# Performance work log

Measured on AMD Instinct MI355X. Metric: run time of the kernel, lower is better.

## Reference

```python
import jax, jax.numpy as jnp
import numpy as np

E = 8        # num_experts
D_IN = 512   # num_inputs
H = 256      # num_neurons_expert
T = 64       # num_neurons_tower
B = 16384    # batch


def setup_inputs() -> dict:
    key = jax.random.key(0)
    ks = jax.random.split(key, 7)
    s_in = 1.0 / np.sqrt(D_IN)
    s_h = 1.0 / np.sqrt(H)
    return {
        "xv": jax.random.normal(ks[0], (B, D_IN), dtype=jnp.float32),
        # expert weights stacked: torch Linear weight is (out,in) -> (E, H, D_IN)
        "We": jax.random.uniform(ks[1], (E, H, D_IN), jnp.float32, -s_in, s_in),
        "be": jax.random.uniform(ks[2], (E, H), jnp.float32, -s_in, s_in),
        "Wg": jax.random.uniform(ks[3], (E, D_IN), jnp.float32, -s_in, s_in),
        "bg": jax.random.uniform(ks[4], (E,), jnp.float32, -s_in, s_in),
        "Wt": jax.random.uniform(ks[5], (T, H), jnp.float32, -s_h, s_h),
        "bt": jax.random.uniform(ks[6], (T,), jnp.float32, -s_h, s_h),
    }


def reference(xv, We, be, Wg, bg, Wt, bt):
    # All experts as one batched GEMM: [B,D] x [E,H,D] -> [B,E,H]
    experts = jax.nn.relu(jnp.einsum("bd,ehd->beh", xv, We) + be[None, :, :])
    # Dropout is identity in eval mode.
    gate = jax.nn.softmax(xv @ Wg.T + bg, axis=1)            # [B,E]
    combined = jnp.einsum("beh,be->bh", experts, gate)        # [B,H]
    out = jax.nn.sigmoid(combined @ Wt.T + bt)                # [B,T]
    return out
```

## Files before the change

### kernel.cpp

```cpp
#include <hip/hip_runtime.h>
#include <hip/hip_bf16.h>
#include <stdint.h>

typedef unsigned short u16;
typedef __bf16 bf16x8 __attribute__((ext_vector_type(8)));
typedef float f32x4 __attribute__((ext_vector_type(4)));

#define LDS_A_USH 8192
#define LDS_B_USH 16384

__device__ __forceinline__ void glds16(const void* g, void* l) {
  __builtin_amdgcn_global_load_lds(
      (const __attribute__((address_space(1))) unsigned int*)g,
      (__attribute__((address_space(3))) unsigned int*)l, 16, 0, 0);
}

__device__ __forceinline__ u16 f2bf(float f) {
  unsigned int u = __builtin_bit_cast(unsigned int, f);
  u += 0x7fffu + ((u >> 16) & 1u);
  return (u16)(u >> 16);
}

__global__ __launch_bounds__(256) void prep_kernel(
    const float* __restrict__ xv, const float* __restrict__ We,
    const float* __restrict__ Wg, const float* __restrict__ bg,
    const float* __restrict__ Wt,
    u16* __restrict__ xv_bf, u16* __restrict__ We_bf,
    u16* __restrict__ Wt_bf, float* __restrict__ gate) {
  const int bx = blockIdx.x;
  if (bx < 4096) {
    const int wid = threadIdx.x >> 6, lane = threadIdx.x & 63;
    const int row = bx * 4 + wid;
    const float* xr = xv + (row << 9) + lane * 8;
    float4 x0 = *(const float4*)xr;
    float4 x1 = *(const float4*)(xr + 4);
    uint4 o;
    o.x = (unsigned)f2bf(x0.x) | ((unsigned)f2bf(x0.y) << 16);
    o.y = (unsigned)f2bf(x0.z) | ((unsigned)f2bf(x0.w) << 16);
    o.z = (unsigned)f2bf(x1.x) | ((unsigned)f2bf(x1.y) << 16);
    o.w = (unsigned)f2bf(x1.z) | ((unsigned)f2bf(x1.w) << 16);
    *(uint4*)(xv_bf + (row << 9) + lane * 8) = o;
    float s[8];
#pragma unroll
    for (int e = 0; e < 8; e++) {
      const float* wg = Wg + (e << 9) + lane * 8;
      float4 w0 = *(const float4*)wg;
      float4 w1 = *(const float4*)(wg + 4);
      s[e] = x0.x * w0.x + x0.y * w0.y + x0.z * w0.z + x0.w * w0.w +
             x1.x * w1.x + x1.y * w1.y + x1.z * w1.z + x1.w * w1.w;
    }
#pragma unroll
    for (int e = 0; e < 8; e++) {
#pragma unroll
      for (int off = 32; off > 0; off >>= 1) s[e] += __shfl_xor(s[e], off);
      s[e] += bg[e];
    }
    float mx = s[0];
#pragma unroll
    for (int e = 1; e < 8; e++) mx = fmaxf(mx, s[e]);
    float p[8], sum = 0.f;
#pragma unroll
    for (int e = 0; e < 8; e++) { p[e] = __expf(s[e] - mx); sum += p[e]; }
    float inv = 1.f / sum;
    if (lane == 0) {
      float4 g0 = {p[0] * inv, p[1] * inv, p[2] * inv, p[3] * inv};
      float4 g1 = {p[4] * inv, p[5] * inv, p[6] * inv, p[7] * inv};
      *(float4*)(gate + row * 8) = g0;
      *(float4*)(gate + row * 8 + 4) = g1;
    }
  } else {
    const int base = (bx - 4096) * 2048 + threadIdx.x * 8;
    const float* src;
    u16* dst;
    if (base < 1048576) { src = We + base; dst = We_bf + base; }
    else { src = Wt + (base - 1048576); dst = Wt_bf + (base - 1048576); }
    float4 a = *(const float4*)src;
    float4 b = *(const float4*)(src + 4);
    uint4 o;
    o.x = (unsigned)f2bf(a.x) | ((unsigned)f2bf(a.y) << 16);
    o.y = (unsigned)f2bf(a.z) | ((unsigned)f2bf(a.w) << 16);
    o.z = (unsigned)f2bf(b.x) | ((unsigned)f2bf(b.y) << 16);
    o.w = (unsigned)f2bf(b.z) | ((unsigned)f2bf(b.w) << 16);
    *(uint4*)dst = o;
  }
}

__global__ __launch_bounds__(256, 2) void moe_main(
    const u16* __restrict__ xv_bf, const u16* __restrict__ We_bf,
    const float* __restrict__ be, const float* __restrict__ gate,
    const u16* __restrict__ Wt_bf, float* __restrict__ part) {
  __shared__ u16 lds[LDS_A_USH + LDS_B_USH];

  const int bx = blockIdx.x;
  const int mb = bx >> 1;
  const int hb = bx & 1;
  const int m0 = mb << 6;
  const int tid = threadIdx.x;
  const int lane = tid & 63;
  const int wid = tid >> 6;
  const int wm = wid >> 1;
  const int wn = wid & 1;
  const int l15 = lane & 15;
  const int l4 = lane >> 4;

  f32x4 comb[2][4];
#pragma unroll
  for (int mt = 0; mt < 2; mt++)
#pragma unroll
    for (int nt = 0; nt < 4; nt++) comb[mt][nt] = {0.f, 0.f, 0.f, 0.f};

  for (int e = 0; e < 8; e++) {
    f32x4 acc[2][4];
#pragma unroll
    for (int mt = 0; mt < 2; mt++)
#pragma unroll
      for (int nt = 0; nt < 4; nt++) acc[mt][nt] = {0.f, 0.f, 0.f, 0.f};

    const u16* Wb = We_bf + (e << 17);
    for (int kc = 0; kc < 4; kc++) {
      __syncthreads();
      const int kofs = kc << 7;
#pragma unroll
      for (int r = 0; r < 4; r++) {
        int gi = r * 256 + tid;
        int m = gi >> 4, s = gi & 15;
        int g = (s & 8) | ((s & 7) ^ (m & 7));
        glds16(xv_bf + ((m0 + m) << 9) + kofs + (g << 3), &lds[gi << 3]);
      }
#pragma unroll
      for (int r = 0; r < 8; r++) {
        int gi = r * 256 + tid;
        int n = gi >> 4, s = gi & 15;
        int g = (s & 8) | ((s & 7) ^ (n & 7));
        glds16(Wb + (((hb << 7) + n) << 9) + kofs + (g << 3),
               &lds[LDS_A_USH + (gi << 3)]);
      }
      __syncthreads();
#pragma unroll
      for (int ks = 0; ks < 4; ks++) {
        const int gg = ks * 4 + l4;
        bf16x8 af[2], bfr[4];
#pragma unroll
        for (int mt = 0; mt < 2; mt++) {
          int row = wm * 32 + mt * 16 + l15;
          int slot = (gg & 8) | ((gg & 7) ^ (row & 7));
          af[mt] = *(const bf16x8*)&lds[(row << 7) + (slot << 3)];
        }
#pragma unroll
        for (int nt = 0; nt < 4; nt++) {
          int n = wn * 64 + nt * 16 + l15;
          int slot = (gg & 8) | ((gg & 7) ^ (n & 7));
          bfr[nt] = *(const bf16x8*)&lds[LDS_A_USH + (n << 7) + (slot << 3)];
        }
#pragma unroll
        for (int mt = 0; mt < 2; mt++)
#pragma unroll
          for (int nt = 0; nt < 4; nt++)
            acc[mt][nt] = __builtin_amdgcn_mfma_f32_16x16x32_bf16(
                af[mt], bfr[nt], acc[mt][nt], 0, 0, 0);
      }
    }
    float bev[4];
#pragma unroll
    for (int nt = 0; nt < 4; nt++)
      bev[nt] = be[(e << 8) + (hb << 7) + wn * 64 + nt * 16 + l15];
#pragma unroll
    for (int mt = 0; mt < 2; mt++) {
#pragma unroll
      for (int i = 0; i < 4; i++) {
        float g = gate[((m0 + wm * 32 + mt * 16 + l4 * 4 + i) << 3) + e];
#pragma unroll
        for (int nt = 0; nt < 4; nt++)
          comb[mt][nt][i] += g * fmaxf(acc[mt][nt][i] + bev[nt], 0.f);
      }
    }
  }

  __syncthreads();
#pragma unroll
  for (int mt = 0; mt < 2; mt++)
#pragma unroll
    for (int i = 0; i < 4; i++) {
      int row = wm * 32 + mt * 16 + l4 * 4 + i;
#pragma unroll
      for (int nt = 0; nt < 4; nt++) {
        int col = wn * 64 + nt * 16 + l15;
        __bf16 v = (__bf16)comb[mt][nt][i];
        lds[row * 136 + col] = __builtin_bit_cast(u16, v);
      }
    }
  __syncthreads();
  f32x4 tacc[4];
#pragma unroll
  for (int nt = 0; nt < 4; nt++) tacc[nt] = {0.f, 0.f, 0.f, 0.f};
  const u16* WtB = Wt_bf + (hb << 7);
#pragma unroll
  for (int kc = 0; kc < 4; kc++) {
    int ko = kc * 32 + l4 * 8;
    bf16x8 aT = *(const bf16x8*)&lds[(wid * 16 + l15) * 136 + ko];
#pragma unroll
    for (int nt = 0; nt < 4; nt++) {
      bf16x8 bT = *(const bf16x8*)&WtB[(nt * 16 + l15) * 256 + ko];
      tacc[nt] = __builtin_amdgcn_mfma_f32_16x16x32_bf16(aT, bT, tacc[nt], 0, 0, 0);
    }
  }
  float* pout = part + hb * 1048576;
#pragma unroll
  for (int nt = 0; nt < 4; nt++)
#pragma unroll
    for (int i = 0; i < 4; i++) {
      int grow = m0 + wid * 16 + l4 * 4 + i;
      pout[grow * 64 + nt * 16 + l15] = tacc[nt][i];
    }
}

__global__ __launch_bounds__(256) void finish_kernel(
    const float* __restrict__ part, const float* __restrict__ bt,
    float* __restrict__ out) {
  const int idx = (blockIdx.x * 256 + threadIdx.x) << 2;
  float4 a = *(const float4*)(part + idx);
  float4 b = *(const float4*)(part + 1048576 + idx);
  float4 c = *(const float4*)(bt + (idx & 63));
  float4 r;
  r.x = 1.f / (1.f + __expf(-(a.x + b.x + c.x)));
  r.y = 1.f / (1.f + __expf(-(a.y + b.y + c.y)));
  r.z = 1.f / (1.f + __expf(-(a.z + b.z + c.z)));
  r.w = 1.f / (1.f + __expf(-(a.w + b.w + c.w)));
  *(float4*)(out + idx) = r;
}

extern "C" void kernel_launch(void* const* d_in, const int* in_sizes, int n_in,
                              void* d_out, int out_size, void* d_ws, size_t ws_size,
                              hipStream_t stream) {
  const float* xv = (const float*)d_in[0];
  const float* We = (const float*)d_in[1];
  const float* be = (const float*)d_in[2];
  const float* Wg = (const float*)d_in[3];
  const float* bg = (const float*)d_in[4];
  const float* Wt = (const float*)d_in[5];
  const float* bt = (const float*)d_in[6];

  char* ws = (char*)d_ws;
  u16* xv_bf = (u16*)ws;
  u16* We_bf = (u16*)(ws + 16777216);
  u16* Wt_bf = (u16*)(ws + 18874368);
  float* gate = (float*)(ws + 18907136);
  float* part = (float*)(ws + 19431424);

  prep_kernel<<<4616, 256, 0, stream>>>(xv, We, Wg, bg, Wt, xv_bf, We_bf, Wt_bf, gate);
  moe_main<<<512, 256, 0, stream>>>(xv_bf, We_bf, be, gate, Wt_bf, part);
  finish_kernel<<<1024, 256, 0, stream>>>(part, bt, (float*)d_out);
}
```

Measured before the change: 154.2 us.

## Fuse gating, x conversion and tower output into a single double-buffered MoE kernel

Removes the separate xv-to-bf16 pass and the finish kernel. Each 512-thread block now holds its 64-row x tile in registers as bf16, computes the gate on the MFMA units with a split hi/lo bf16 scheme, and double-buffers the expert weight chunks in LDS. The block also computes all 256 hidden columns and applies the tower bias and sigmoid directly. This cuts global traffic for the bf16 x copy, the gate array and the partial sums, and overlaps weight loads with compute. In exchange the grid shrinks to 256 blocks with heavy register use, which may limit occupancy on a 256-CU GPU.

```diff
diff --git a/kernel.cpp b/kernel.cpp
--- a/kernel.cpp
+++ b/kernel.cpp
@@ -6,8 +6,6 @@
 typedef __bf16 bf16x8 __attribute__((ext_vector_type(8)));
 typedef float f32x4 __attribute__((ext_vector_type(4)));
 
-#define LDS_A_USH 8192
-#define LDS_B_USH 16384
 
 __device__ __forceinline__ void glds16(const void* g, void* l) {
   __builtin_amdgcn_global_load_lds(
@@ -21,59 +19,16 @@
   return (u16)(u >> 16);
 }
 
-__global__ __launch_bounds__(256) void prep_kernel(
-    const float* __restrict__ xv, const float* __restrict__ We,
-    const float* __restrict__ Wg, const float* __restrict__ bg,
-    const float* __restrict__ Wt,
-    u16* __restrict__ xv_bf, u16* __restrict__ We_bf,
-    u16* __restrict__ Wt_bf, float* __restrict__ gate) {
+__global__ __launch_bounds__(256) void prep_w(
+    const float* __restrict__ We, const float* __restrict__ Wt,
+    const float* __restrict__ Wg,
+    u16* __restrict__ We_bf, u16* __restrict__ Wt_bf,
+    u16* __restrict__ Wg_hi, u16* __restrict__ Wg_lo) {
   const int bx = blockIdx.x;
-  if (bx < 4096) {
-    const int wid = threadIdx.x >> 6, lane = threadIdx.x & 63;
-    const int row = bx * 4 + wid;
-    const float* xr = xv + (row << 9) + lane * 8;
-    float4 x0 = *(const float4*)xr;
-    float4 x1 = *(const float4*)(xr + 4);
-    uint4 o;
-    o.x = (unsigned)f2bf(x0.x) | ((unsigned)f2bf(x0.y) << 16);
-    o.y = (unsigned)f2bf(x0.z) | ((unsigned)f2bf(x0.w) << 16);
-    o.z = (unsigned)f2bf(x1.x) | ((unsigned)f2bf(x1.y) << 16);
-    o.w = (unsigned)f2bf(x1.z) | ((unsigned)f2bf(x1.w) << 16);
-    *(uint4*)(xv_bf + (row << 9) + lane * 8) = o;
-    float s[8];
-#pragma unroll
-    for (int e = 0; e < 8; e++) {
-      const float* wg = Wg + (e << 9) + lane * 8;
-      float4 w0 = *(const float4*)wg;
-      float4 w1 = *(const float4*)(wg + 4);
-      s[e] = x0.x * w0.x + x0.y * w0.y + x0.z * w0.z + x0.w * w0.w +
-             x1.x * w1.x + x1.y * w1.y + x1.z * w1.z + x1.w * w1.w;
-    }
-#pragma unroll
-    for (int e = 0; e < 8; e++) {
-#pragma unroll
-      for (int off = 32; off > 0; off >>= 1) s[e] += __shfl_xor(s[e], off);
-      s[e] += bg[e];
-    }
-    float mx = s[0];
-#pragma unroll
-    for (int e = 1; e < 8; e++) mx = fmaxf(mx, s[e]);
-    float p[8], sum = 0.f;
-#pragma unroll
-    for (int e = 0; e < 8; e++) { p[e] = __expf(s[e] - mx); sum += p[e]; }
-    float inv = 1.f / sum;
-    if (lane == 0) {
-      float4 g0 = {p[0] * inv, p[1] * inv, p[2] * inv, p[3] * inv};
-      float4 g1 = {p[4] * inv, p[5] * inv, p[6] * inv, p[7] * inv};
-      *(float4*)(gate + row * 8) = g0;
-      *(float4*)(gate + row * 8 + 4) = g1;
-    }
-  } else {
-    const int base = (bx - 4096) * 2048 + threadIdx.x * 8;
-    const float* src;
-    u16* dst;
-    if (base < 1048576) { src = We + base; dst = We_bf + base; }
-    else { src = Wt + (base - 1048576); dst = Wt_bf + (base - 1048576); }
+  if (bx < 520) {
+    const float* src; u16* dst;
+    if (bx < 512) { int base = bx * 2048 + threadIdx.x * 8; src = We + base; dst = We_bf + base; }
+    else { int base = (bx - 512) * 2048 + threadIdx.x * 8; src = Wt + base; dst = Wt_bf + base; }
     float4 a = *(const float4*)src;
     float4 b = *(const float4*)(src + 4);
     uint4 o;
@@ -82,26 +37,118 @@
     o.z = (unsigned)f2bf(b.x) | ((unsigned)f2bf(b.y) << 16);
     o.w = (unsigned)f2bf(b.z) | ((unsigned)f2bf(b.w) << 16);
     *(uint4*)dst = o;
-  }
-}
-
-__global__ __launch_bounds__(256, 2) void moe_main(
-    const u16* __restrict__ xv_bf, const u16* __restrict__ We_bf,
-    const float* __restrict__ be, const float* __restrict__ gate,
-    const u16* __restrict__ Wt_bf, float* __restrict__ part) {
-  __shared__ u16 lds[LDS_A_USH + LDS_B_USH];
-
-  const int bx = blockIdx.x;
-  const int mb = bx >> 1;
-  const int hb = bx & 1;
-  const int m0 = mb << 6;
+  } else {
+    int base = (bx - 520) * 2048 + threadIdx.x * 8;
+    float x[8];
+    float4 a = *(const float4*)(Wg + base);
+    float4 b = *(const float4*)(Wg + base + 4);
+    x[0]=a.x; x[1]=a.y; x[2]=a.z; x[3]=a.w; x[4]=b.x; x[5]=b.y; x[6]=b.z; x[7]=b.w;
+    u16 h[8], l[8];
+#pragma unroll
+    for (int j = 0; j < 8; j++) {
+      h[j] = f2bf(x[j]);
+      float hf = __builtin_bit_cast(float, ((unsigned)h[j]) << 16);
+      l[j] = f2bf(x[j] - hf);
+    }
+    uint4 oh, ol;
+    oh.x = (unsigned)h[0] | ((unsigned)h[1] << 16);
+    oh.y = (unsigned)h[2] | ((unsigned)h[3] << 16);
+    oh.z = (unsigned)h[4] | ((unsigned)h[5] << 16);
+    oh.w = (unsigned)h[6] | ((unsigned)h[7] << 16);
+    ol.x = (unsigned)l[0] | ((unsigned)l[1] << 16);
+    ol.y = (unsigned)l[2] | ((unsigned)l[3] << 16);
+    ol.z = (unsigned)l[4] | ((unsigned)l[5] << 16);
+    ol.w = (unsigned)l[6] | ((unsigned)l[7] << 16);
+    *(uint4*)(Wg_hi + base) = oh;
+    *(uint4*)(Wg_lo + base) = ol;
+  }
+}
+
+__device__ __forceinline__ void stage_chunk(const u16* __restrict__ We_bf,
+                                            u16* ldsbuf, int t, int tid) {
+  const int e_ = t >> 2, kc_ = t & 3;
+  const u16* src = We_bf + (e_ << 17) + (kc_ << 7);
+#pragma unroll
+  for (int r = 0; r < 8; r++) {
+    int gi = r * 512 + tid;
+    int n = gi >> 4, s = gi & 15;
+    int g = (s & 8) | ((s & 7) ^ (n & 7));
+    glds16(src + (n << 9) + (g << 3), ldsbuf + (gi << 3));
+  }
+}
+
+__global__ __launch_bounds__(512, 2) void moe_main(
+    const float* __restrict__ xv, const u16* __restrict__ We_bf,
+    const float* __restrict__ be, const float* __restrict__ bg,
+    const u16* __restrict__ Wg_hi, const u16* __restrict__ Wg_lo,
+    const u16* __restrict__ Wt_bf, const float* __restrict__ bt,
+    float* __restrict__ out) {
+  __shared__ u16 lds[65536];
+
   const int tid = threadIdx.x;
   const int lane = tid & 63;
   const int wid = tid >> 6;
-  const int wm = wid >> 1;
-  const int wn = wid & 1;
+  const int wm = wid >> 2;
+  const int wn = wid & 3;
   const int l15 = lane & 15;
   const int l4 = lane >> 4;
+  const int m0 = blockIdx.x << 6;
+
+  stage_chunk(We_bf, lds, 0, tid);
+
+  bf16x8 ah[2][16];
+  f32x4 gacc[2] = {{0.f,0.f,0.f,0.f},{0.f,0.f,0.f,0.f}};
+  const int esrc = l15 & 7;
+#pragma unroll
+  for (int mt = 0; mt < 2; mt++) {
+    bf16x8 alo[16];
+#pragma unroll
+    for (int ks = 0; ks < 16; ks++) {
+      const float* ap = xv + ((m0 + wm * 32 + mt * 16 + l15) << 9) + ks * 32 + l4 * 8;
+      float4 xa = *(const float4*)ap;
+      float4 xb = *(const float4*)(ap + 4);
+      float x[8];
+      x[0]=xa.x; x[1]=xa.y; x[2]=xa.z; x[3]=xa.w; x[4]=xb.x; x[5]=xb.y; x[6]=xb.z; x[7]=xb.w;
+      bf16x8 hv, lv;
+#pragma unroll
+      for (int j = 0; j < 8; j++) {
+        u16 hb_ = f2bf(x[j]);
+        float hf = __builtin_bit_cast(float, ((unsigned)hb_) << 16);
+        hv[j] = __builtin_bit_cast(__bf16, hb_);
+        lv[j] = __builtin_bit_cast(__bf16, f2bf(x[j] - hf));
+      }
+      ah[mt][ks] = hv;
+      alo[ks] = lv;
+    }
+#pragma unroll
+    for (int ks = 0; ks < 16; ks++) {
+      bf16x8 wh = *(const bf16x8*)(Wg_hi + (esrc << 9) + ks * 32 + l4 * 8);
+      bf16x8 wl = *(const bf16x8*)(Wg_lo + (esrc << 9) + ks * 32 + l4 * 8);
+      gacc[mt] = __builtin_amdgcn_mfma_f32_16x16x32_bf16(ah[mt][ks], wh, gacc[mt], 0, 0, 0);
+      gacc[mt] = __builtin_amdgcn_mfma_f32_16x16x32_bf16(alo[ks],    wh, gacc[mt], 0, 0, 0);
+      gacc[mt] = __builtin_amdgcn_mfma_f32_16x16x32_bf16(ah[mt][ks], wl, gacc[mt], 0, 0, 0);
+    }
+  }
+  float gv[2][4];
+  {
+    float bgv = bg[esrc];
+#pragma unroll
+    for (int mt = 0; mt < 2; mt++)
+#pragma unroll
+      for (int i = 0; i < 4; i++) {
+        float z = gacc[mt][i] + bgv;
+        float mx = z;
+        mx = fmaxf(mx, __shfl_xor(mx, 1));
+        mx = fmaxf(mx, __shfl_xor(mx, 2));
+        mx = fmaxf(mx, __shfl_xor(mx, 4));
+        float p = __expf(z - mx);
+        float s = p;
+        s += __shfl_xor(s, 1);
+        s += __shfl_xor(s, 2);
+        s += __shfl_xor(s, 4);
+        gv[mt][i] = p / s;
+      }
+  }
 
   f32x4 comb[2][4];
 #pragma unroll
@@ -109,6 +156,7 @@
 #pragma unroll
     for (int nt = 0; nt < 4; nt++) comb[mt][nt] = {0.f, 0.f, 0.f, 0.f};
 
+#pragma unroll 1
   for (int e = 0; e < 8; e++) {
     f32x4 acc[2][4];
 #pragma unroll
@@ -116,64 +164,43 @@
 #pragma unroll
       for (int nt = 0; nt < 4; nt++) acc[mt][nt] = {0.f, 0.f, 0.f, 0.f};
 
-    const u16* Wb = We_bf + (e << 17);
+#pragma unroll
     for (int kc = 0; kc < 4; kc++) {
       __syncthreads();
-      const int kofs = kc << 7;
-#pragma unroll
-      for (int r = 0; r < 4; r++) {
-        int gi = r * 256 + tid;
-        int m = gi >> 4, s = gi & 15;
-        int g = (s & 8) | ((s & 7) ^ (m & 7));
-        glds16(xv_bf + ((m0 + m) << 9) + kofs + (g << 3), &lds[gi << 3]);
-      }
-#pragma unroll
-      for (int r = 0; r < 8; r++) {
-        int gi = r * 256 + tid;
-        int n = gi >> 4, s = gi & 15;
-        int g = (s & 8) | ((s & 7) ^ (n & 7));
-        glds16(Wb + (((hb << 7) + n) << 9) + kofs + (g << 3),
-               &lds[LDS_A_USH + (gi << 3)]);
-      }
-      __syncthreads();
+      int t = e * 4 + kc + 1;
+      if (t < 32) stage_chunk(We_bf, &lds[(((kc & 1) ^ 1) << 15)], t, tid);
+      const u16* ldsB = &lds[((kc & 1) << 15)];
 #pragma unroll
       for (int ks = 0; ks < 4; ks++) {
         const int gg = ks * 4 + l4;
-        bf16x8 af[2], bfr[4];
-#pragma unroll
-        for (int mt = 0; mt < 2; mt++) {
-          int row = wm * 32 + mt * 16 + l15;
-          int slot = (gg & 8) | ((gg & 7) ^ (row & 7));
-          af[mt] = *(const bf16x8*)&lds[(row << 7) + (slot << 3)];
-        }
+        bf16x8 bfr[4];
 #pragma unroll
         for (int nt = 0; nt < 4; nt++) {
           int n = wn * 64 + nt * 16 + l15;
           int slot = (gg & 8) | ((gg & 7) ^ (n & 7));
-          bfr[nt] = *(const bf16x8*)&lds[LDS_A_USH + (n << 7) + (slot << 3)];
+          bfr[nt] = *(const bf16x8*)&ldsB[(n << 7) + (slot << 3)];
         }
 #pragma unroll
         for (int mt = 0; mt < 2; mt++)
 #pragma unroll
           for (int nt = 0; nt < 4; nt++)
             acc[mt][nt] = __builtin_amdgcn_mfma_f32_16x16x32_bf16(
-                af[mt], bfr[nt], acc[mt][nt], 0, 0, 0);
+                ah[mt][kc * 4 + ks], bfr[nt], acc[mt][nt], 0, 0, 0);
       }
     }
     float bev[4];
 #pragma unroll
     for (int nt = 0; nt < 4; nt++)
-      bev[nt] = be[(e << 8) + (hb << 7) + wn * 64 + nt * 16 + l15];
-#pragma unroll
-    for (int mt = 0; mt < 2; mt++) {
+      bev[nt] = be[(e << 8) + wn * 64 + nt * 16 + l15];
+#pragma unroll
+    for (int mt = 0; mt < 2; mt++)
 #pragma unroll
       for (int i = 0; i < 4; i++) {
-        float g = gate[((m0 + wm * 32 + mt * 16 + l4 * 4 + i) << 3) + e];
+        float g = __shfl(gv[mt][i], (lane & 48) | e);
 #pragma unroll
         for (int nt = 0; nt < 4; nt++)
           comb[mt][nt][i] += g * fmaxf(acc[mt][nt][i] + bev[nt], 0.f);
       }
-    }
   }
 
   __syncthreads();
@@ -186,47 +213,34 @@
       for (int nt = 0; nt < 4; nt++) {
         int col = wn * 64 + nt * 16 + l15;
         __bf16 v = (__bf16)comb[mt][nt][i];
-        lds[row * 136 + col] = __builtin_bit_cast(u16, v);
+        lds[row * 264 + col] = __builtin_bit_cast(u16, v);
       }
     }
   __syncthreads();
-  f32x4 tacc[4];
-#pragma unroll
-  for (int nt = 0; nt < 4; nt++) tacc[nt] = {0.f, 0.f, 0.f, 0.f};
-  const u16* WtB = Wt_bf + (hb << 7);
-#pragma unroll
-  for (int kc = 0; kc < 4; kc++) {
-    int ko = kc * 32 + l4 * 8;
-    bf16x8 aT = *(const bf16x8*)&lds[(wid * 16 + l15) * 136 + ko];
+  if (wid < 4) {
+    f32x4 tacc[4];
+#pragma unroll
+    for (int nt = 0; nt < 4; nt++) tacc[nt] = {0.f, 0.f, 0.f, 0.f};
+#pragma unroll
+    for (int ks = 0; ks < 8; ks++) {
+      bf16x8 aT = *(const bf16x8*)&lds[(wid * 16 + l15) * 264 + ks * 32 + l4 * 8];
+#pragma unroll
+      for (int nt = 0; nt < 4; nt++) {
+        bf16x8 bT = *(const bf16x8*)&Wt_bf[(nt * 16 + l15) * 256 + ks * 32 + l4 * 8];
+        tacc[nt] = __builtin_amdgcn_mfma_f32_16x16x32_bf16(aT, bT, tacc[nt], 0, 0, 0);
+      }
+    }
 #pragma unroll
     for (int nt = 0; nt < 4; nt++) {
-      bf16x8 bT = *(const bf16x8*)&WtB[(nt * 16 + l15) * 256 + ko];
-      tacc[nt] = __builtin_amdgcn_mfma_f32_16x16x32_bf16(aT, bT, tacc[nt], 0, 0, 0);
-    }
-  }
-  float* pout = part + hb * 1048576;
-#pragma unroll
-  for (int nt = 0; nt < 4; nt++)
-#pragma unroll
-    for (int i = 0; i < 4; i++) {
-      int grow = m0 + wid * 16 + l4 * 4 + i;
-      pout[grow * 64 + nt * 16 + l15] = tacc[nt][i];
-    }
-}
-
-__global__ __launch_bounds__(256) void finish_kernel(
-    const float* __restrict__ part, const float* __restrict__ bt,
-    float* __restrict__ out) {
-  const int idx = (blockIdx.x * 256 + threadIdx.x) << 2;
-  float4 a = *(const float4*)(part + idx);
-  float4 b = *(const float4*)(part + 1048576 + idx);
-  float4 c = *(const float4*)(bt + (idx & 63));
-  float4 r;
-  r.x = 1.f / (1.f + __expf(-(a.x + b.x + c.x)));
-  r.y = 1.f / (1.f + __expf(-(a.y + b.y + c.y)));
-  r.z = 1.f / (1.f + __expf(-(a.z + b.z + c.z)));
-  r.w = 1.f / (1.f + __expf(-(a.w + b.w + c.w)));
-  *(float4*)(out + idx) = r;
+      float btv = bt[nt * 16 + l15];
+#pragma unroll
+      for (int i = 0; i < 4; i++) {
+        int row = m0 + wid * 16 + l4 * 4 + i;
+        float v = tacc[nt][i] + btv;
+        out[row * 64 + nt * 16 + l15] = 1.f / (1.f + __expf(-v));
+      }
+    }
+  }
 }
 
 extern "C" void kernel_launch(void* const* d_in, const int* in_sizes, int n_in,
@@ -241,13 +255,12 @@
   const float* bt = (const float*)d_in[6];
 
   char* ws = (char*)d_ws;
-  u16* xv_bf = (u16*)ws;
-  u16* We_bf = (u16*)(ws + 16777216);
-  u16* Wt_bf = (u16*)(ws + 18874368);
-  float* gate = (float*)(ws + 18907136);
-  float* part = (float*)(ws + 19431424);
-
-  prep_kernel<<<4616, 256, 0, stream>>>(xv, We, Wg, bg, Wt, xv_bf, We_bf, Wt_bf, gate);
-  moe_main<<<512, 256, 0, stream>>>(xv_bf, We_bf, be, gate, Wt_bf, part);
-  finish_kernel<<<1024, 256, 0, stream>>>(part, bt, (float*)d_out);
-}
+  u16* We_bf = (u16*)ws;
+  u16* Wt_bf = (u16*)(ws + 2097152);
+  u16* Wg_hi = (u16*)(ws + 2129920);
+  u16* Wg_lo = (u16*)(ws + 2138112);
+
+  prep_w<<<522, 256, 0, stream>>>(We, Wt, Wg, We_bf, Wt_bf, Wg_hi, Wg_lo);
+  moe_main<<<256, 512, 0, stream>>>(xv, We_bf, be, bg, Wg_hi, Wg_lo, Wt_bf, bt,
+                                    (float*)d_out);
+}
```

Measured after the change: 165.8 us. 7.6% more time.
